# Optimization experiments

Measured on AMD Instinct MI355X. Metric: run time of the kernel, lower is better.

## Reference

```python
import jax, jax.numpy as jnp
import numpy as np

B, S, D_MODEL, D_INNER = 64, 128, 1024, 1024


def setup_inputs() -> dict:
    key = jax.random.key(0)
    ks = jax.random.split(key, 10)
    sc = 0.02
    return {
        "embeddings": jax.random.normal(ks[0], (B, S, D_MODEL), dtype=jnp.float32),
        "Wq": jax.random.normal(ks[1], (D_MODEL, D_INNER), dtype=jnp.float32) * sc,
        "bq": jnp.zeros((D_INNER,), dtype=jnp.float32),
        "Wk": jax.random.normal(ks[2], (D_MODEL, D_INNER), dtype=jnp.float32) * sc,
        "bk": jnp.zeros((D_INNER,), dtype=jnp.float32),
        "Wv": jax.random.normal(ks[3], (D_MODEL, D_INNER), dtype=jnp.float32) * sc,
        "bv": jnp.zeros((D_INNER,), dtype=jnp.float32),
        "w": jax.random.normal(ks[4], (S, S), dtype=jnp.float32) * sc,
        "Wo": jax.random.normal(ks[5], (D_INNER, D_MODEL), dtype=jnp.float32) * sc,
        "bo": jnp.zeros((D_MODEL,), dtype=jnp.float32),
    }


def reference(embeddings, Wq, bq, Wk, bk, Wv, bv, w, Wo, bo):
    # embeddings: [B, S, Dm]
    seq_len = embeddings.shape[1]
    q = embeddings @ Wq + bq          # [B, S, Di]
    k = embeddings @ Wk + bk
    v = embeddings @ Wv + bv

    max_k = jnp.max(k, axis=1, keepdims=True)   # [B, 1, Di]
    exp_k = jnp.exp(k - max_k)                  # [B, S, Di]

    max_w = jnp.max(w, axis=1, keepdims=True)   # [S, 1]
    wn = w - max_w                              # [S, S]
    tril = jnp.tril(jnp.ones((seq_len, seq_len), dtype=bool))
    wn = jnp.where(tril, wn[:seq_len, :seq_len], -jnp.inf)
    # torch.einsum('bjj,bjd->bjd', exp_w, x) picks the DIAGONAL of exp_w
    # (repeated subscript j) and multiplies elementwise along the seq dim.
    diag_w = jnp.exp(jnp.diagonal(wn))          # [S]; tril diagonal is True so finite
    dw = diag_w[None, :, None]                  # [1, S, 1]

    numerator = dw * (exp_k * v)                # [B, S, Di]
    denominator = dw * exp_k                    # [B, S, Di]
    out = jax.nn.sigmoid(q) * (numerator / denominator)
    return out @ Wo + bo                        # [B, S, Dm]
```

## Files before the change

kernel.cpp:

```cpp
#include <hip/hip_runtime.h>


typedef short bf16x8 __attribute__((ext_vector_type(8)));
typedef float f32x4  __attribute__((ext_vector_type(4)));

__device__ __forceinline__ short f2bf(float f) {
  union { float f; unsigned u; } x; x.f = f;
  unsigned r = x.u + 0x7fffu + ((x.u >> 16) & 1u);
  return (short)(r >> 16);
}

struct alignas(16) S8 { short v[8]; };

#define GLDS(g, l) \
  __builtin_amdgcn_global_load_lds((const __attribute__((address_space(1))) void*)(g), \
                                   (__attribute__((address_space(3))) void*)(l), 16, 0, 0)
#define BAR()    __builtin_amdgcn_s_barrier()
#define PRIO(x)  __builtin_amdgcn_s_setprio(x)
#define VMCNT(N) asm volatile("s_waitcnt vmcnt(" #N ")" ::: "memory")
#define LGKM0()  asm volatile("s_waitcnt lgkmcnt(0)" ::: "memory")
#define MFMA(a, b, c) __builtin_amdgcn_mfma_f32_16x16x32_bf16((a), (b), (c), 0, 0, 0)

__global__ __launch_bounds__(256) void prep_kernel(
    const float* __restrict__ emb, const float* __restrict__ Wq, const float* __restrict__ Wv,
    const float* __restrict__ Wo, short* __restrict__ embB, short* __restrict__ WqvT,
    short* __restrict__ WoT) {
  __shared__ float tr[64 * 65];
  const int t = threadIdx.x;
  const int bid = blockIdx.x;
  const int gdim = gridDim.x;

  for (size_t i = (size_t)bid * 256 + t; i < 1048576; i += (size_t)gdim * 256) {
    const float4* p = (const float4*)emb + i * 2;
    float4 a = p[0], b = p[1];
    S8 s;
    s.v[0] = f2bf(a.x); s.v[1] = f2bf(a.y); s.v[2] = f2bf(a.z); s.v[3] = f2bf(a.w);
    s.v[4] = f2bf(b.x); s.v[5] = f2bf(b.y); s.v[6] = f2bf(b.z); s.v[7] = f2bf(b.w);
    ((S8*)embB)[i] = s;
  }

  const int rr = t >> 4, cc4 = (t & 15) * 4;
  const int orow = t >> 3, ocol8 = (t & 7) * 8;
  for (int z = bid; z < 768; z += gdim) {
    const float* in; short* op; int ti;
    if (z < 256)      { in = Wq; op = WqvT;           ti = z; }
    else if (z < 512) { in = Wv; op = WqvT + 1048576; ti = z - 256; }
    else              { in = Wo; op = WoT;            ti = z - 512; }
    const int bx = (ti & 15) * 64, by = (ti >> 4) * 64;
    __syncthreads();
#pragma unroll
    for (int k = 0; k < 4; ++k) {
      float4 v = *(const float4*)&in[(size_t)(by + rr + 16 * k) * 1024 + bx + cc4];
      float* d = &tr[(rr + 16 * k) * 65 + cc4];
      d[0] = v.x; d[1] = v.y; d[2] = v.z; d[3] = v.w;
    }
    __syncthreads();
#pragma unroll
    for (int h = 0; h < 2; ++h) {
      const int oc = orow + 32 * h;
      S8 s;
#pragma unroll
      for (int i = 0; i < 8; ++i) s.v[i] = f2bf(tr[(ocol8 + i) * 65 + oc]);
      *(S8*)&op[(size_t)(bx + oc) * 1024 + by + ocol8] = s;
    }
  }
}

__global__ __launch_bounds__(512, 2) void gemm_qv_kernel(
    const short* __restrict__ A, const short* __restrict__ BT,
    const float* __restrict__ bq, const float* __restrict__ bv, short* __restrict__ X) {
  __shared__ short As[2][256 * 64];
  __shared__ short Bqs[2][128 * 64];
  __shared__ short Bvs[2][128 * 64];
  const int t = threadIdx.x;
  const int lane = t & 63;
  const int w = t >> 6;
  const int l16 = lane & 15;
  const int quad = lane >> 4;
  const int b = blockIdx.x;
  const int wg = (b & 7) * 32 + (b >> 3);
  const int bm = (wg >> 3) * 256;
  const int bn = (wg & 7) * 128;
  const int wm = (w & 3) * 64;
  const int wn = (w >> 2) * 64;

  const int r8 = t >> 3;
  const int swe = ((t & 7) ^ (r8 & 7)) * 8;
  const short* gA = A + (size_t)(bm + r8) * 1024 + swe;
  const short* gq = BT + (size_t)(bn + r8) * 1024 + swe;
  const short* gv = BT + (size_t)(1024 + bn + r8) * 1024 + swe;
  short* lA = &As[0][0] + w * 512;
  short* lq = &Bqs[0][0] + w * 512;
  short* lv = &Bvs[0][0] + w * 512;

#define QV_STAGE(k, s) do {                                             \
    const short* a_ = gA + (k) * 64; short* la_ = lA + (s) * 16384;     \
    GLDS(a_, la_);               GLDS(a_ + 64 * 1024, la_ + 4096);      \
    GLDS(a_ + 128 * 1024, la_ + 8192); GLDS(a_ + 192 * 1024, la_ + 12288); \
    const short* q_ = gq + (k) * 64; short* lq_ = lq + (s) * 8192;      \
    GLDS(q_, lq_);               GLDS(q_ + 64 * 1024, lq_ + 4096);      \
    const short* v_ = gv + (k) * 64; short* lv_ = lv + (s) * 8192;      \
    GLDS(v_, lv_);               GLDS(v_ + 64 * 1024, lv_ + 4096);      \
  } while (0)

  const int csw0 = (quad ^ (l16 & 7)) * 8;
  const int csw1 = ((quad + 4) ^ (l16 & 7)) * 8;
  const short* fA0 = &As[0][0] + (wm + l16) * 64 + csw0;
  const short* fA1 = &As[0][0] + (wm + l16) * 64 + csw1;
  const short* fq0 = &Bqs[0][0] + (wn + l16) * 64 + csw0;
  const short* fq1 = &Bqs[0][0] + (wn + l16) * 64 + csw1;
  const short* fv0 = &Bvs[0][0] + (wn + l16) * 64 + csw0;
  const short* fv1 = &Bvs[0][0] + (wn + l16) * 64 + csw1;

  f32x4 aq[4][4] = {};
  f32x4 av[4][4] = {};

  QV_STAGE(0, 0);
  QV_STAGE(1, 1);

  for (int j = 0; j < 16; ++j) {
    const int s = j & 1;
    const short* sA0 = fA0 + s * 16384;
    const short* sA1 = fA1 + s * 16384;
    const short* sq0 = fq0 + s * 8192;
    const short* sq1 = fq1 + s * 8192;
    const short* sv0 = fv0 + s * 8192;
    const short* sv1 = fv1 + s * 8192;

    if (j < 15) { VMCNT(8); } else { VMCNT(0); }
    BAR();

    {
      bf16x8 a0[4], bq0[4], bv0[4];
#pragma unroll
      for (int i = 0; i < 4; ++i) {
        a0[i] = *(const bf16x8*)(sA0 + i * 1024);
        bq0[i] = *(const bf16x8*)(sq0 + i * 1024);
        bv0[i] = *(const bf16x8*)(sv0 + i * 1024);
      }
      PRIO(1);
#pragma unroll
      for (int i = 0; i < 4; ++i)
#pragma unroll
        for (int n = 0; n < 4; ++n) {
          aq[i][n] = MFMA(a0[i], bq0[n], aq[i][n]);
          av[i][n] = MFMA(a0[i], bv0[n], av[i][n]);
        }
      PRIO(0);
    }
    {
      bf16x8 a1[4], bq1[4], bv1[4];
#pragma unroll
      for (int i = 0; i < 4; ++i) {
        a1[i] = *(const bf16x8*)(sA1 + i * 1024);
        bq1[i] = *(const bf16x8*)(sq1 + i * 1024);
        bv1[i] = *(const bf16x8*)(sv1 + i * 1024);
      }
      PRIO(1);
#pragma unroll
      for (int i = 0; i < 4; ++i)
#pragma unroll
        for (int n = 0; n < 4; ++n) {
          aq[i][n] = MFMA(a1[i], bq1[n], aq[i][n]);
          av[i][n] = MFMA(a1[i], bv1[n], av[i][n]);
        }
      PRIO(0);
    }

    LGKM0();
    BAR();
    if (j < 14) QV_STAGE(j + 2, s);
  }
#undef QV_STAGE

#pragma unroll
  for (int n = 0; n < 4; ++n) {
    const int col = bn + wn + n * 16 + l16;
    const float bql = bq[col], bvl = bv[col];
#pragma unroll
    for (int i = 0; i < 4; ++i)
#pragma unroll
      for (int r = 0; r < 4; ++r) {
        const int row = bm + wm + i * 16 + quad * 4 + r;
        const float q = aq[i][n][r] + bql;
        const float v = av[i][n][r] + bvl;
        const float sg = 1.0f / (1.0f + __expf(-q));
        X[(size_t)row * 1024 + col] = f2bf(sg * v);
      }
  }
}

__global__ __launch_bounds__(256) void gemm_bt_kernel(
    const short* __restrict__ A, const short* __restrict__ BT, float* __restrict__ C,
    const float* __restrict__ bias) {
  __shared__ short As[128 * 64];
  __shared__ short Bs[128 * 64];
  const int t = threadIdx.x;
  const int lane = t & 63;
  const int w = t >> 6;
  const int l16 = lane & 15;
  const int quad = lane >> 4;
  const int bm = blockIdx.x * 128;
  const int bn = blockIdx.y * 128;
  const int wm = (w & 1) * 64;
  const int wn = (w >> 1) * 64;

  const int r8 = t >> 3;
  const int swe = ((t & 7) ^ (r8 & 7)) * 8;
  const short* pA0 = A + (size_t)(bm + r8) * 1024 + swe;
  const short* pA1 = pA0 + 32 * 1024;
  const short* pA2 = pA0 + 64 * 1024;
  const short* pA3 = pA0 + 96 * 1024;
  const short* pB0 = BT + (size_t)(bn + r8) * 1024 + swe;
  const short* pB1 = pB0 + 32 * 1024;
  const short* pB2 = pB0 + 64 * 1024;
  const short* pB3 = pB0 + 96 * 1024;
  short* lA = As + w * 512;
  short* lB = Bs + w * 512;

  const int qsw0 = (quad ^ (l16 & 7)) * 8;
  const int qsw1 = ((quad + 4) ^ (l16 & 7)) * 8;
  const short* fA0 = As + (wm + l16) * 64 + qsw0;
  const short* fA1 = As + (wm + l16) * 64 + qsw1;
  const short* fB0 = Bs + (wn + l16) * 64 + qsw0;
  const short* fB1 = Bs + (wn + l16) * 64 + qsw1;

  f32x4 acc[4][4] = {};

  for (int it = 0; it < 16; ++it) {
    GLDS(pA0, lA); GLDS(pA1, lA + 2048); GLDS(pA2, lA + 4096); GLDS(pA3, lA + 6144);
    GLDS(pB0, lB); GLDS(pB1, lB + 2048); GLDS(pB2, lB + 4096); GLDS(pB3, lB + 6144);
    pA0 += 64; pA1 += 64; pA2 += 64; pA3 += 64;
    pB0 += 64; pB1 += 64; pB2 += 64; pB3 += 64;
    __syncthreads();

#pragma unroll
    for (int h = 0; h < 2; h++) {
      const short* fA = h ? fA1 : fA0;
      const short* fB = h ? fB1 : fB0;
      bf16x8 av[4], bw[4];
#pragma unroll
      for (int i = 0; i < 4; i++) av[i] = *(const bf16x8*)(fA + i * 1024);
#pragma unroll
      for (int j = 0; j < 4; j++) bw[j] = *(const bf16x8*)(fB + j * 1024);
#pragma unroll
      for (int i = 0; i < 4; i++)
#pragma unroll
        for (int j = 0; j < 4; j++)
          acc[i][j] = MFMA(av[i], bw[j], acc[i][j]);
    }
    __syncthreads();
  }

#pragma unroll
  for (int j = 0; j < 4; j++) {
    int col = bn + wn + j * 16 + l16;
    float bl = bias[col];
#pragma unroll
    for (int i = 0; i < 4; i++)
#pragma unroll
      for (int r = 0; r < 4; r++) {
        int row = bm + wm + i * 16 + quad * 4 + r;
        C[(size_t)row * 1024 + col] = acc[i][j][r] + bl;
      }
  }
}

extern "C" void kernel_launch(void* const* d_in, const int* in_sizes, int n_in,
                              void* d_out, int out_size, void* d_ws, size_t ws_size,
                              hipStream_t stream) {
  const float* emb = (const float*)d_in[0];
  const float* Wq  = (const float*)d_in[1];
  const float* bq  = (const float*)d_in[2];
  const float* Wv  = (const float*)d_in[5];
  const float* bv  = (const float*)d_in[6];
  const float* Wo  = (const float*)d_in[8];
  const float* bo  = (const float*)d_in[9];
  float* out = (float*)d_out;

  char* ws = (char*)d_ws;
  short* embB = (short*)(ws);
  short* X    = (short*)(ws + 16777216);
  short* WqvT = (short*)(ws + 33554432);
  short* WoT  = (short*)(ws + 37748736);

  prep_kernel<<<768, 256, 0, stream>>>(emb, Wq, Wv, Wo, embB, WqvT, WoT);
  gemm_qv_kernel<<<256, 512, 0, stream>>>(embB, WqvT, bq, bv, X);
  gemm_bt_kernel<<<dim3(64, 8), 256, 0, stream>>>(X, WoT, out, bo);
}
```

Baseline: 164.1 us.

## Shrink QV GEMM tiles to 128x128, K=32 with triple-buffered LDS pipeline

```diff
diff --git a/kernel.cpp b/kernel.cpp
--- a/kernel.cpp
+++ b/kernel.cpp
@@ -66,51 +66,49 @@
   }
 }
 
-__global__ __launch_bounds__(512, 2) void gemm_qv_kernel(
+__global__ __launch_bounds__(256, 2) void gemm_qv_kernel(
     const short* __restrict__ A, const short* __restrict__ BT,
     const float* __restrict__ bq, const float* __restrict__ bv, short* __restrict__ X) {
-  __shared__ short As[2][256 * 64];
-  __shared__ short Bqs[2][128 * 64];
-  __shared__ short Bvs[2][128 * 64];
+  __shared__ short As[3][128 * 32];
+  __shared__ short Bqs[3][128 * 32];
+  __shared__ short Bvs[3][128 * 32];
   const int t = threadIdx.x;
   const int lane = t & 63;
   const int w = t >> 6;
   const int l16 = lane & 15;
   const int quad = lane >> 4;
   const int b = blockIdx.x;
-  const int wg = (b & 7) * 32 + (b >> 3);
-  const int bm = (wg >> 3) * 256;
+  const int wg = (b & 7) * 64 + (b >> 3);
+  const int bm = (wg >> 3) * 128;
   const int bn = (wg & 7) * 128;
-  const int wm = (w & 3) * 64;
-  const int wn = (w >> 2) * 64;
-
-  const int r8 = t >> 3;
-  const int swe = ((t & 7) ^ (r8 & 7)) * 8;
-  const short* gA = A + (size_t)(bm + r8) * 1024 + swe;
-  const short* gq = BT + (size_t)(bn + r8) * 1024 + swe;
-  const short* gv = BT + (size_t)(1024 + bn + r8) * 1024 + swe;
+  const int wm = (w & 1) * 64;
+  const int wn = (w >> 1) * 64;
+
+  const int sr = t >> 2;
+  const int swk = ((t & 3) ^ ((t >> 3) & 3)) * 8;
+  const short* pA0 = A + (size_t)(bm + sr) * 1024 + swk;
+  const short* pA1 = pA0 + 64 * 1024;
+  const short* pQ0 = BT + (size_t)(bn + sr) * 1024 + swk;
+  const short* pQ1 = pQ0 + 64 * 1024;
+  const short* pV0 = BT + (size_t)(1024 + bn + sr) * 1024 + swk;
+  const short* pV1 = pV0 + 64 * 1024;
   short* lA = &As[0][0] + w * 512;
   short* lq = &Bqs[0][0] + w * 512;
   short* lv = &Bvs[0][0] + w * 512;
 
-#define QV_STAGE(k, s) do {                                             \
-    const short* a_ = gA + (k) * 64; short* la_ = lA + (s) * 16384;     \
-    GLDS(a_, la_);               GLDS(a_ + 64 * 1024, la_ + 4096);      \
-    GLDS(a_ + 128 * 1024, la_ + 8192); GLDS(a_ + 192 * 1024, la_ + 12288); \
-    const short* q_ = gq + (k) * 64; short* lq_ = lq + (s) * 8192;      \
-    GLDS(q_, lq_);               GLDS(q_ + 64 * 1024, lq_ + 4096);      \
-    const short* v_ = gv + (k) * 64; short* lv_ = lv + (s) * 8192;      \
-    GLDS(v_, lv_);               GLDS(v_ + 64 * 1024, lv_ + 4096);      \
+#define QV_STAGE(kk, s) do {                                                  \
+    GLDS(pA0 + (kk) * 32, lA + (s) * 4096);                                   \
+    GLDS(pA1 + (kk) * 32, lA + (s) * 4096 + 2048);                            \
+    GLDS(pQ0 + (kk) * 32, lq + (s) * 4096);                                   \
+    GLDS(pQ1 + (kk) * 32, lq + (s) * 4096 + 2048);                            \
+    GLDS(pV0 + (kk) * 32, lv + (s) * 4096);                                   \
+    GLDS(pV1 + (kk) * 32, lv + (s) * 4096 + 2048);                            \
   } while (0)
 
-  const int csw0 = (quad ^ (l16 & 7)) * 8;
-  const int csw1 = ((quad + 4) ^ (l16 & 7)) * 8;
-  const short* fA0 = &As[0][0] + (wm + l16) * 64 + csw0;
-  const short* fA1 = &As[0][0] + (wm + l16) * 64 + csw1;
-  const short* fq0 = &Bqs[0][0] + (wn + l16) * 64 + csw0;
-  const short* fq1 = &Bqs[0][0] + (wn + l16) * 64 + csw1;
-  const short* fv0 = &Bvs[0][0] + (wn + l16) * 64 + csw0;
-  const short* fv1 = &Bvs[0][0] + (wn + l16) * 64 + csw1;
+  const int csw = (quad ^ ((l16 >> 1) & 3)) * 8;
+  const short* fA = &As[0][0] + (wm + l16) * 32 + csw;
+  const short* fQ = &Bqs[0][0] + (wn + l16) * 32 + csw;
+  const short* fV = &Bvs[0][0] + (wn + l16) * 32 + csw;
 
   f32x4 aq[4][4] = {};
   f32x4 av[4][4] = {};
@@ -118,58 +116,33 @@
   QV_STAGE(0, 0);
   QV_STAGE(1, 1);
 
-  for (int j = 0; j < 16; ++j) {
-    const int s = j & 1;
-    const short* sA0 = fA0 + s * 16384;
-    const short* sA1 = fA1 + s * 16384;
-    const short* sq0 = fq0 + s * 8192;
-    const short* sq1 = fq1 + s * 8192;
-    const short* sv0 = fv0 + s * 8192;
-    const short* sv1 = fv1 + s * 8192;
-
-    if (j < 15) { VMCNT(8); } else { VMCNT(0); }
+  for (int j = 0; j < 32; ++j) {
+    const int s = j % 3;
+    if (j < 31) { VMCNT(6); } else { VMCNT(0); }
     BAR();
-
-    {
-      bf16x8 a0[4], bq0[4], bv0[4];
-#pragma unroll
-      for (int i = 0; i < 4; ++i) {
-        a0[i] = *(const bf16x8*)(sA0 + i * 1024);
-        bq0[i] = *(const bf16x8*)(sq0 + i * 1024);
-        bv0[i] = *(const bf16x8*)(sv0 + i * 1024);
+    if (j < 30) QV_STAGE(j + 2, (j + 2) % 3);
+
+    const short* sA = fA + s * 4096;
+    const short* sQ = fQ + s * 4096;
+    const short* sV = fV + s * 4096;
+    bf16x8 a[4], bqf[4], bvf[4];
+#pragma unroll
+    for (int i = 0; i < 4; ++i) {
+      a[i] = *(const bf16x8*)(sA + i * 512);
+      bqf[i] = *(const bf16x8*)(sQ + i * 512);
+      bvf[i] = *(const bf16x8*)(sV + i * 512);
+    }
+    PRIO(1);
+#pragma unroll
+    for (int i = 0; i < 4; ++i)
+#pragma unroll
+      for (int n = 0; n < 4; ++n) {
+        aq[i][n] = MFMA(a[i], bqf[n], aq[i][n]);
+        av[i][n] = MFMA(a[i], bvf[n], av[i][n]);
       }
-      PRIO(1);
-#pragma unroll
-      for (int i = 0; i < 4; ++i)
-#pragma unroll
-        for (int n = 0; n < 4; ++n) {
-          aq[i][n] = MFMA(a0[i], bq0[n], aq[i][n]);
-          av[i][n] = MFMA(a0[i], bv0[n], av[i][n]);
-        }
-      PRIO(0);
-    }
-    {
-      bf16x8 a1[4], bq1[4], bv1[4];
-#pragma unroll
-      for (int i = 0; i < 4; ++i) {
-        a1[i] = *(const bf16x8*)(sA1 + i * 1024);
-        bq1[i] = *(const bf16x8*)(sq1 + i * 1024);
-        bv1[i] = *(const bf16x8*)(sv1 + i * 1024);
-      }
-      PRIO(1);
-#pragma unroll
-      for (int i = 0; i < 4; ++i)
-#pragma unroll
-        for (int n = 0; n < 4; ++n) {
-          aq[i][n] = MFMA(a1[i], bq1[n], aq[i][n]);
-          av[i][n] = MFMA(a1[i], bv1[n], av[i][n]);
-        }
-      PRIO(0);
-    }
-
+    PRIO(0);
     LGKM0();
     BAR();
-    if (j < 14) QV_STAGE(j + 2, s);
   }
 #undef QV_STAGE
 
@@ -285,6 +258,6 @@
   short* WoT  = (short*)(ws + 37748736);
 
   prep_kernel<<<768, 256, 0, stream>>>(emb, Wq, Wv, Wo, embB, WqvT, WoT);
-  gemm_qv_kernel<<<256, 512, 0, stream>>>(embB, WqvT, bq, bv, X);
+  gemm_qv_kernel<<<512, 256, 0, stream>>>(embB, WqvT, bq, bv, X);
   gemm_bt_kernel<<<dim3(64, 8), 256, 0, stream>>>(X, WoT, out, bo);
 }
```

Result: slower. 167.5 us (+2.0%).
